# Kernel optimization log

Hardware: AMD Instinct MI355X
Metric: run time of the kernel (lower is better)

The kernel has to match this reference:

```python
import jax, jax.numpy as jnp
import numpy as np

B, IN_DIM, N, L = 8, 2, 512, 64
D_MODEL = 32
D_FF = 32          # must equal D_MODEL: output_bn is BatchNorm2d(d_model) applied to skip
DEPTH = 3          # blocks=3 * layers=1; dilation resets to 1 each block -> all dilations = 1
KS = 2             # temporal kernel size
EPS = 1e-5         # BatchNorm eps


def setup_inputs() -> dict:
    key = jax.random.key(0)
    ks = jax.random.split(key, 16)
    s = 0.1  # weight scale for numeric sanity
    x = jax.random.normal(ks[0], (B, IN_DIM, N, L), jnp.float32)
    a = jax.random.uniform(ks[1], (N, N), jnp.float32)
    adj = a / a.sum(axis=1, keepdims=True)  # row-stochastic diffusion matrix
    return {
        "x": x,
        "adj": adj,
        "Wstart": jax.random.normal(ks[2], (D_MODEL, IN_DIM), jnp.float32) * s,
        "bstart": jnp.zeros((D_MODEL,), jnp.float32),
        "Wf": jax.random.normal(ks[3], (DEPTH, D_MODEL, D_MODEL, KS), jnp.float32) * s,
        "bf": jnp.zeros((DEPTH, D_MODEL), jnp.float32),
        "Wg": jax.random.normal(ks[4], (DEPTH, D_MODEL, D_MODEL, KS), jnp.float32) * s,
        "bg": jnp.zeros((DEPTH, D_MODEL), jnp.float32),
        "Wskip": jax.random.normal(ks[5], (DEPTH, D_FF, D_MODEL), jnp.float32) * s,
        "bskip": jnp.zeros((DEPTH, D_FF), jnp.float32),
        "Wgc": jax.random.normal(ks[6], (DEPTH, D_MODEL, 3 * D_MODEL), jnp.float32) * s,
        "bgc": jnp.zeros((DEPTH, D_MODEL), jnp.float32),
        "gcbn_g": jnp.ones((DEPTH, D_MODEL), jnp.float32),
        "gcbn_b": jnp.zeros((DEPTH, D_MODEL), jnp.float32),
        "bn_g": jnp.ones((DEPTH, D_MODEL), jnp.float32),
        "bn_b": jnp.zeros((DEPTH, D_MODEL), jnp.float32),
        "obn_g": jnp.ones((D_MODEL,), jnp.float32),
        "obn_b": jnp.zeros((D_MODEL,), jnp.float32),
    }


def _c1x1(x, W, b):
    # Conv2d with (1,1) kernel == channel mixing. x: [b,c,n,l], W: [o,c]
    return jnp.einsum('bcnl,oc->bonl', x, W) + b[None, :, None, None]


def _dconv(x, W, b, d):
    # Conv2d kernel (1,2), dilation d along time (valid). W: [o,c,2]
    Lx = x.shape[-1]
    y = (jnp.einsum('bcnl,oc->bonl', x[..., :Lx - d], W[..., 0])
         + jnp.einsum('bcnl,oc->bonl', x[..., d:], W[..., 1]))
    return y + b[None, :, None, None]


def _bn(x, g, bta):
    # eval-mode BatchNorm2d: running_mean=0, running_var=1
    inv = g / jnp.sqrt(1.0 + EPS)
    return x * inv[None, :, None, None] + bta[None, :, None, None]


def reference(x, adj, Wstart, bstart, Wf, bf, Wg, bg, Wskip, bskip,
              Wgc, bgc, gcbn_g, gcbn_b, bn_g, bn_b, obn_g, obn_b):
    rf = 1 + DEPTH * (KS - 1)  # receptive field with dilation 1 per layer
    h = _c1x1(x, Wstart, bstart)
    if h.shape[-1] < rf:
        h = jnp.pad(h, ((0, 0), (0, 0), (0, 0), (rf - h.shape[-1], 0)))
    skip = None
    for i in range(DEPTH):
        residual = h
        filt = jnp.tanh(_dconv(h, Wf[i], bf[i], 1))
        gate = jax.nn.sigmoid(_dconv(h, Wg[i], bg[i], 1))
        h = filt * gate
        s = _c1x1(h, Wskip[i], bskip[i])
        skip = s if skip is None else s + skip[..., -s.shape[-1]:]
        if i == DEPTH - 1:
            break
        # order-2 graph diffusion: h, A h, A^2 h -> concat -> 1x1 conv -> BN (dropout: eval noop)
        x1 = jnp.einsum('bcnl,nm->bcml', h, adj)
        x2 = jnp.einsum('bcnl,nm->bcml', x1, adj)
        cat = jnp.concatenate([h, x1, x2], axis=1)
        g = _bn(_c1x1(cat, Wgc[i], bgc[i]), gcbn_g[i], gcbn_b[i])
        h = g + residual[..., -g.shape[-1]:]
        h = _bn(h, bn_g[i], bn_b[i])
    out = _bn(skip, obn_g, obn_b)
    return jnp.swapaxes(out, 1, 3)  # [B, L', N, C]
```

## Files before the change

### kernel.cpp

```cpp
#include <hip/hip_runtime.h>
#include <hip/hip_bf16.h>

#define B_     8
#define CIN_   2
#define N_     512
#define C_     32
#define L_     64
#define LOUT_  61
#define BUF_   ((size_t)(8*32*512*64))

typedef __hip_bfloat16 bf16;
typedef unsigned short ushort_t;
typedef unsigned int u32;
typedef __attribute__((ext_vector_type(8))) unsigned short us8;
typedef __attribute__((ext_vector_type(8))) short bf16x8;
typedef __attribute__((ext_vector_type(4))) float f32x4;

static __device__ __forceinline__ float bits2f(ushort_t u) {
    return __uint_as_float(((unsigned)u) << 16);
}
static __device__ __forceinline__ ushort_t f2bits(float v) {
    unsigned u = __float_as_uint(v);
    return (ushort_t)((u + 0x7fffu + ((u >> 16) & 1u)) >> 16);
}

static __device__ __forceinline__ void gload16(const ushort_t* g, ushort_t* l) {
    __builtin_amdgcn_global_load_lds(
        (const __attribute__((address_space(1))) unsigned int*)g,
        (__attribute__((address_space(3))) unsigned int*)l,
        16, 0, 0);
}

static __device__ __forceinline__ u32 swap1(u32 v) {
    return (u32)__builtin_amdgcn_update_dpp(0, (int)v, 0xB1, 0xF, 0xF, true);
}

__global__ void k_start(const float* __restrict__ x,
                        const float* __restrict__ Wst,
                        const float* __restrict__ bst,
                        ushort_t* __restrict__ h) {
    int idx = blockIdx.x * 256 + threadIdx.x;
    int l0 = (idx & 7) * 8;
    int n  = (idx >> 3) & 511;
    int o  = (idx >> 12) & 31;
    int b  = idx >> 17;
    float w0 = Wst[o * 2], w1 = Wst[o * 2 + 1], bb = bst[o];
    int xbase = (b * CIN_ * N_ + n) * L_ + l0;
    float va[8], vb[8];
    *(float4*)&va[0] = *(const float4*)(x + xbase);
    *(float4*)&va[4] = *(const float4*)(x + xbase + 4);
    *(float4*)&vb[0] = *(const float4*)(x + xbase + N_ * L_);
    *(float4*)&vb[4] = *(const float4*)(x + xbase + N_ * L_ + 4);
    us8 r;
    #pragma unroll
    for (int k = 0; k < 8; ++k) r[k] = f2bits(bb + va[k] * w0 + vb[k] * w1);
    *(us8*)(h + (size_t)idx * 8) = r;
}

__global__ void k_transA(const float* __restrict__ adj, ushort_t* __restrict__ adjT) {
    __shared__ float buf[64][65];
    int ti = blockIdx.x & 7;
    int tj = blockIdx.x >> 3;
    int t = threadIdx.x;
    for (int r = 0; r < 16; ++r) {
        int e = t + 256 * r;
        int rl = e >> 6, cl = e & 63;
        buf[rl][cl] = adj[(size_t)(ti * 64 + rl) * 512 + tj * 64 + cl];
    }
    __syncthreads();
    for (int r = 0; r < 16; ++r) {
        int e = t + 256 * r;
        int ml = e >> 6, nl = e & 63;
        adjT[(size_t)(tj * 64 + ml) * 512 + ti * 64 + nl] = f2bits(buf[nl][ml]);
    }
}

__global__ __launch_bounds__(256, 2) void k_sq(const ushort_t* __restrict__ adjT,
                                               ushort_t* __restrict__ adj2T) {
    __shared__ __align__(16) ushort_t lds2[8192];
    ushort_t* As = lds2;
    ushort_t* Bs = lds2 + 4096;
    int mt = blockIdx.x & 7, nc = blockIdx.x >> 3;
    int t = threadIdx.x, lane = t & 63, w = t >> 6;
    int la = lane & 15, q = lane >> 4;
    f32x4 acc[4];
    #pragma unroll
    for (int mi = 0; mi < 4; ++mi) acc[mi] = (f32x4)0.f;
    for (int p0 = 0; p0 < 512; p0 += 64) {
        __syncthreads();
        #pragma unroll
        for (int r = 0; r < 2; ++r) {
            int e = t + 256 * r, ml = e >> 3, oct = e & 7;
            int sw = ((oct + (ml >> 3)) & 7) << 3;
            *(us8*)(As + ml * 64 + sw) =
                *(const us8*)(adjT + (size_t)(mt * 64 + ml) * 512 + p0 + oct * 8);
            *(us8*)(Bs + ml * 64 + sw) =
                *(const us8*)(adjT + (size_t)(p0 + ml) * 512 + nc * 64 + oct * 8);
        }
        __syncthreads();
        #pragma unroll
        for (int ks = 0; ks < 2; ++ks) {
            bf16x8 a[4];
            #pragma unroll
            for (int mi = 0; mi < 4; ++mi) {
                int m = mi * 16 + la;
                int bl = (ks * 4 + q + (m >> 3)) & 7;
                a[mi] = *(const bf16x8*)(As + m * 64 + bl * 8);
            }
            bf16x8 bv;
            {
                int n = w * 16 + la;
                int rot = ((n >> 3) + ks * 4 + q) & 7;
                int col = rot * 8 + (n & 7);
                const ushort_t* p = Bs + (ks * 32 + q * 8) * 64 + col;
                #pragma unroll
                for (int j = 0; j < 8; ++j) bv[j] = (short)p[j * 64];
            }
            #pragma unroll
            for (int mi = 0; mi < 4; ++mi)
                acc[mi] = __builtin_amdgcn_mfma_f32_16x16x32_bf16(a[mi], bv, acc[mi], 0, 0, 0);
        }
    }
    __syncthreads();
    ushort_t* Ys = lds2;
    #pragma unroll
    for (int mi = 0; mi < 4; ++mi)
        #pragma unroll
        for (int r = 0; r < 4; ++r)
            Ys[(mi * 16 + q * 4 + r) * 72 + w * 16 + la] = f2bits(acc[mi][r]);
    __syncthreads();
    #pragma unroll
    for (int r = 0; r < 2; ++r) {
        int e = t + 256 * r, ml = e >> 3, oct = e & 7;
        us8 v = *(const us8*)(Ys + ml * 72 + oct * 8);
        *(us8*)(adj2T + (size_t)(mt * 64 + ml) * 512 + nc * 64 + oct * 8) = v;
    }
}

__global__ __launch_bounds__(256, 2) void k_gs_mfma(
        const ushort_t* __restrict__ h,
        const float* __restrict__ Wf, const float* __restrict__ bfp,
        const float* __restrict__ Wg, const float* __restrict__ bgp,
        const float* __restrict__ Wsk, const float* __restrict__ bsk,
        ushort_t* __restrict__ G, float* __restrict__ out,
        int off, int mode, int storeG,
        const float* __restrict__ og, const float* __restrict__ obb) {
    __shared__ __align__(16) ushort_t Hs[128 * 72];
    __shared__ __align__(16) ushort_t Asf[32 * 72];
    __shared__ __align__(16) ushort_t Asg[32 * 72];
    __shared__ __align__(16) ushort_t As2[32 * 40];
    __shared__ float bfv[32], bgv[32], bsv[32];
    int t = threadIdx.x;
    int b = blockIdx.x >> 7, n0 = (blockIdx.x & 127) * 4;
    int lane = t & 63, w = t >> 6;
    int la = lane & 15, q = lane >> 4;

    {
        int o = t >> 3, k8 = (t & 7) * 8;
        us8 vf, vg;
        #pragma unroll
        for (int i = 0; i < 8; ++i) {
            int k = k8 + i, c = k & 31, tap = k >> 5;
            vf[i] = f2bits(Wf[o * 64 + c * 2 + tap]);
            vg[i] = f2bits(Wg[o * 64 + c * 2 + tap]);
        }
        *(us8*)(Asf + o * 72 + k8) = vf;
        *(us8*)(Asg + o * 72 + k8) = vg;
        if (k8 < 32) {
            us8 vs;
            #pragma unroll
            for (int i = 0; i < 8; ++i) vs[i] = f2bits(Wsk[o * 32 + k8 + i]);
            *(us8*)(As2 + o * 40 + k8) = vs;
        }
        if (t < 32) { bfv[t] = bfp[t]; bgv[t] = bgp[t]; bsv[t] = bsk[t]; }
    }
    const ushort_t* hb = h + (size_t)(b * 32) * 512 * 64;
    #pragma unroll
    for (int r = 0; r < 4; ++r) {
        int e = t + 256 * r;
        int row = e >> 3, oct = e & 7;
        us8 v = *(const us8*)(hb + ((size_t)(row >> 2) * 512 + n0 + (row & 3)) * 64 + oct * 8);
        int sw = (oct + row + (row >> 5)) & 7;
        *(us8*)(Hs + row * 72 + sw * 8) = v;
    }
    {
        int row = t >> 1, hf = t & 1;
        *(uint2*)(Hs + row * 72 + 64 + hf * 4) = make_uint2(0u, 0u);
    }
    __syncthreads();

    bf16x8 af[2][2], ag[2][2];
    #pragma unroll
    for (int mt = 0; mt < 2; ++mt)
        #pragma unroll
        for (int ks = 0; ks < 2; ++ks) {
            af[mt][ks] = *(const bf16x8*)(Asf + (mt * 16 + la) * 72 + ks * 32 + q * 8);
            ag[mt][ks] = *(const bf16x8*)(Asg + (mt * 16 + la) * 72 + ks * 32 + q * 8);
        }

    f32x4 fa[2][4], ga[2][4];
    #pragma unroll
    for (int mt = 0; mt < 2; ++mt)
        #pragma unroll
        for (int ct = 0; ct < 4; ++ct) { fa[mt][ct] = (f32x4)0.f; ga[mt][ct] = (f32x4)0.f; }
    #pragma unroll
    for (int ct = 0; ct < 4; ++ct) {
        #pragma unroll
        for (int ks = 0; ks < 2; ++ks) {
            int le = ct * 16 + la + ks;
            bf16x8 bv;
            #pragma unroll
            for (int j = 0; j < 8; ++j) {
                int row = 32 * q + 4 * j + w;
                int pos = (le < 64) ? ((((le >> 3) + row + q) & 7) * 8 + (le & 7)) : le;
                bv[j] = (short)Hs[row * 72 + pos];
            }
            #pragma unroll
            for (int mt = 0; mt < 2; ++mt) {
                fa[mt][ct] = __builtin_amdgcn_mfma_f32_16x16x32_bf16(af[mt][ks], bv, fa[mt][ct], 0, 0, 0);
                ga[mt][ct] = __builtin_amdgcn_mfma_f32_16x16x32_bf16(ag[mt][ks], bv, ga[mt][ct], 0, 0, 0);
            }
        }
    }

    #pragma unroll
    for (int mt = 0; mt < 2; ++mt)
        #pragma unroll
        for (int ct = 0; ct < 4; ++ct)
            #pragma unroll
            for (int r = 0; r < 4; ++r) {
                int o = mt * 16 + q * 4 + r;
                float fv = fa[mt][ct][r] + bfv[o];
                float gv = ga[mt][ct][r] + bgv[o];
                float ef = __expf(2.f * fv);
                float act = (1.f - 2.f / (ef + 1.f)) * (1.f / (1.f + __expf(-gv)));
                int l = ct * 16 + la;
                int row = o * 4 + w;
                int sw = ((l >> 3) + row + (row >> 5)) & 7;
                Hs[row * 72 + sw * 8 + (l & 7)] = f2bits(act);
            }

    bf16x8 a2[2];
    a2[0] = *(const bf16x8*)(As2 + la * 40 + q * 8);
    a2[1] = *(const bf16x8*)(As2 + (16 + la) * 40 + q * 8);
    f32x4 sa[2][4];
    #pragma unroll
    for (int mt = 0; mt < 2; ++mt)
        #pragma unroll
        for (int ct = 0; ct < 4; ++ct) sa[mt][ct] = (f32x4)0.f;
    #pragma unroll
    for (int ct = 0; ct < 4; ++ct) {
        int le = ct * 16 + la + off;
        bf16x8 bv;
        #pragma unroll
        for (int j = 0; j < 8; ++j) {
            int row = 32 * q + 4 * j + w;
            int pos = (le < 64) ? ((((le >> 3) + row + q) & 7) * 8 + (le & 7)) : le;
            bv[j] = (short)Hs[row * 72 + pos];
        }
        sa[0][ct] = __builtin_amdgcn_mfma_f32_16x16x32_bf16(a2[0], bv, sa[0][ct], 0, 0, 0);
        sa[1][ct] = __builtin_amdgcn_mfma_f32_16x16x32_bf16(a2[1], bv, sa[1][ct], 0, 0, 0);
    }
    __syncthreads();

    if (storeG) {
        #pragma unroll
        for (int r = 0; r < 4; ++r) {
            int e = t + 256 * r;
            int row = e >> 3, oct = e & 7;
            int sw = (oct + row + (row >> 5)) & 7;
            us8 v = *(const us8*)(Hs + row * 72 + sw * 8);
            *(us8*)(G + ((size_t)(b * 32 + (row >> 2)) * 512 + n0 + (row & 3)) * 64 + oct * 8) = v;
        }
    }
    __syncthreads();

    float* St = (float*)Hs;
    const float rbn = rsqrtf(1.f + 1e-5f);
    #pragma unroll
    for (int half = 0; half < 2; ++half) {
        if ((w >> 1) == half) {
            #pragma unroll
            for (int mt = 0; mt < 2; ++mt)
                #pragma unroll
                for (int ct = 0; ct < 4; ++ct) {
                    int col = (w & 1) * 64 + ct * 16 + la;
                    int ob = mt * 16 + q * 4;
                    float4 sv = make_float4(sa[mt][ct][0] + bsv[ob],
                                            sa[mt][ct][1] + bsv[ob + 1],
                                            sa[mt][ct][2] + bsv[ob + 2],
                                            sa[mt][ct][3] + bsv[ob + 3]);
                    *(float4*)(St + col * 36 + ob) = sv;
                }
        }
        __syncthreads();
        {
            int col = t >> 1, o0 = (t & 1) * 16;
            int nr = half * 2 + (col >> 6), l = col & 63;
            if (l < LOUT_) {
                float* po = out + ((size_t)(b * LOUT_ + l) * 512 + n0 + nr) * 32 + o0;
                #pragma unroll
                for (int i = 0; i < 4; ++i) {
                    float4 s = *(float4*)(St + col * 36 + o0 + i * 4);
                    if (mode == 0) {
                        *(float4*)(po + i * 4) = s;
                    } else {
                        float4 old = *(float4*)(po + i * 4);
                        float4 vv = make_float4(old.x + s.x, old.y + s.y,
                                                old.z + s.z, old.w + s.w);
                        if (mode == 2) {
                            int ob = o0 + i * 4;
                            vv.x = vv.x * (og[ob] * rbn) + obb[ob];
                            vv.y = vv.y * (og[ob + 1] * rbn) + obb[ob + 1];
                            vv.z = vv.z * (og[ob + 2] * rbn) + obb[ob + 2];
                            vv.w = vv.w * (og[ob + 3] * rbn) + obb[ob + 3];
                        }
                        *(float4*)(po + i * 4) = vv;
                    }
                }
            }
        }
        __syncthreads();
    }
}

__global__ __launch_bounds__(256, 2) void k_diffuse2(
        const ushort_t* __restrict__ X, const ushort_t* __restrict__ adjT,
        const ushort_t* __restrict__ adj2T,
        ushort_t* __restrict__ Y1, ushort_t* __restrict__ Y2) {
    __shared__ __align__(16) ushort_t lds[32768];
    int cp = blockIdx.x & 15;
    int mt = (blockIdx.x >> 4) & 7;
    int b  = blockIdx.x >> 7;
    int t  = threadIdx.x;
    int lane = t & 63, w = t >> 6;
    int c_loc = w & 1, lh = w >> 1;
    int m0 = mt * 64;
    int la = lane & 15, q = lane >> 4;
    int p_ = la & 1;
    u32 sel = p_ ? 0x07060302u : 0x05040100u;
    const ushort_t* Xb = X + (size_t)(b * 32 + cp * 2) * 512 * 64;
    f32x4 acc1[4][2], acc2[4][2];
    #pragma unroll
    for (int mi = 0; mi < 4; ++mi)
        #pragma unroll
        for (int li = 0; li < 2; ++li) { acc1[mi][li] = (f32x4)0.f; acc2[mi][li] = (f32x4)0.f; }

    union U { u32 u[4]; bf16x8 v; };

    auto STAGE = [&](int n0, ushort_t* bb) {
        ushort_t* As1b = bb;
        ushort_t* As2b = bb + 4096;
        ushort_t* Xsb  = bb + 8192;
        #pragma unroll
        for (int r = 0; r < 2; ++r) {
            int e = t + 256 * r, ml = e >> 3, s = e & 7;
            int og = ((s - (ml >> 3)) & 7) * 8;
            gload16(adjT  + (size_t)(m0 + ml) * 512 + n0 + og, As1b + (size_t)e * 8);
            gload16(adj2T + (size_t)(m0 + ml) * 512 + n0 + og, As2b + (size_t)e * 8);
        }
        #pragma unroll
        for (int r = 0; r < 4; ++r) {
            int e = t + 256 * r;
            int cl = e >> 9, nl = (e >> 3) & 63, s = e & 7;
            int og = ((s - nl - (nl >> 3)) & 7) * 8;
            gload16(Xb + ((size_t)cl * 512 + n0 + nl) * 64 + og, Xsb + (size_t)e * 8);
        }
    };

    STAGE(0, lds);
    __syncthreads();

    for (int it = 0; it < 8; ++it) {
        ushort_t* cur = lds + (it & 1) * 16384;
        if (it < 7) STAGE((it + 1) * 64, lds + ((it + 1) & 1) * 16384);
        ushort_t* As1 = cur;
        ushort_t* As2 = cur + 4096;
        ushort_t* Xs  = cur + 8192;
        const ushort_t* xc = Xs + c_loc * 4096;
        #pragma unroll
        for (int ks = 0; ks < 2; ++ks) {
            bf16x8 a1[4], a2v[4];
            #pragma unroll
            for (int mi = 0; mi < 4; ++mi) {
                int m = mi * 16 + la;
                int bl = (ks * 4 + q + (m >> 3)) & 7;
                a1[mi]  = *(const bf16x8*)(As1 + m * 64 + bl * 8);
                a2v[mi] = *(const bf16x8*)(As2 + m * 64 + bl * 8);
            }
            bf16x8 bb[2];
            #pragma unroll
            for (int li = 0; li < 2; ++li) {
                int l2 = lh * 32 + li * 16 + (la & ~1);
                int r0 = ks * 32 + q * 8 + p_ * 4;
                int brot = ((l2 >> 3) + p_ * 4 + ks * 4 + q) & 7;
                u32 o0 = *(const u32*)(xc + (r0 + 0) * 64 + (((brot + 0) & 7) << 3) + (l2 & 7));
                u32 o1 = *(const u32*)(xc + (r0 + 1) * 64 + (((brot + 1) & 7) << 3) + (l2 & 7));
                u32 o2 = *(const u32*)(xc + (r0 + 2) * 64 + (((brot + 2) & 7) << 3) + (l2 & 7));
                u32 o3 = *(const u32*)(xc + (r0 + 3) * 64 + (((brot + 3) & 7) << 3) + (l2 & 7));
                u32 s0 = swap1(o0), s1 = swap1(o1), s2 = swap1(o2), s3 = swap1(o3);
                u32 lo0 = p_ ? s0 : o0, lo1 = p_ ? s1 : o1;
                u32 lo2 = p_ ? s2 : o2, lo3 = p_ ? s3 : o3;
                u32 hi0 = p_ ? o0 : s0, hi1 = p_ ? o1 : s1;
                u32 hi2 = p_ ? o2 : s2, hi3 = p_ ? o3 : s3;
                U u;
                u.u[0] = __builtin_amdgcn_perm(lo1, lo0, sel);
                u.u[1] = __builtin_amdgcn_perm(lo3, lo2, sel);
                u.u[2] = __builtin_amdgcn_perm(hi1, hi0, sel);
                u.u[3] = __builtin_amdgcn_perm(hi3, hi2, sel);
                bb[li] = u.v;
            }
            #pragma unroll
            for (int mi = 0; mi < 4; ++mi)
                #pragma unroll
                for (int li = 0; li < 2; ++li) {
                    acc1[mi][li] = __builtin_amdgcn_mfma_f32_16x16x32_bf16(a1[mi],  bb[li], acc1[mi][li], 0, 0, 0);
                    acc2[mi][li] = __builtin_amdgcn_mfma_f32_16x16x32_bf16(a2v[mi], bb[li], acc2[mi][li], 0, 0, 0);
                }
        }
        __syncthreads();
    }

    ushort_t* Ys = lds;
    #pragma unroll
    for (int pass = 0; pass < 2; ++pass) {
        __syncthreads();
        f32x4 (*src)[2] = pass ? acc2 : acc1;
        #pragma unroll
        for (int mi = 0; mi < 4; ++mi)
            #pragma unroll
            for (int li = 0; li < 2; ++li)
                #pragma unroll
                for (int r = 0; r < 4; ++r) {
                    int row = mi * 16 + q * 4 + r;
                    int col = lh * 32 + li * 16 + la;
                    Ys[c_loc * 4608 + row * 72 + col] = f2bits(src[mi][li][r]);
                }
        __syncthreads();
        ushort_t* Yo = pass ? Y2 : Y1;
        int c = t >> 7, mrem = t & 127;
        int m = mrem >> 1, lq = mrem & 1;
        #pragma unroll
        for (int r = 0; r < 4; ++r) {
            int l0 = lq * 32 + r * 8;
            us8 v = *(const us8*)(Ys + c * 4608 + m * 72 + l0);
            *(us8*)(Yo + ((size_t)(b * 32 + cp * 2 + c) * 512 + m0 + m) * 64 + l0) = v;
        }
    }
}

__global__ __launch_bounds__(256, 2) void k_gc3_mfma(
        ushort_t* __restrict__ G, const ushort_t* __restrict__ X1,
        const ushort_t* __restrict__ X2, const ushort_t* __restrict__ hres,
        const float* __restrict__ Wgc, const float* __restrict__ bgc,
        const float* __restrict__ gg, const float* __restrict__ gb,
        const float* __restrict__ bg2, const float* __restrict__ bb2) {
    __shared__ __align__(16) ushort_t cat[384 * 72];
    __shared__ __align__(16) ushort_t hr[128 * 64];
    __shared__ __align__(16) ushort_t Aw[32 * 104];
    __shared__ float prm[5][32];
    int t = threadIdx.x;
    int b = blockIdx.x >> 7, n0 = (blockIdx.x & 127) * 4;
    int lane = t & 63, w = t >> 6;
    int la = lane & 15, q = lane >> 4;

    #pragma unroll
    for (int r = 0; r < 12; ++r) {
        int e = t + 256 * r;
        int row = e >> 3, oct = e & 7;
        int k = row >> 2;
        const ushort_t* src = (k < 32) ? G : ((k < 64) ? X1 : X2);
        us8 v = *(const us8*)(src + ((size_t)(b * 32 + (k & 31)) * 512 + n0 + (row & 3)) * 64 + oct * 8);
        int sw = (oct + row + (row >> 5)) & 7;
        *(us8*)(cat + row * 72 + sw * 8) = v;
    }
    #pragma unroll
    for (int r = 0; r < 4; ++r) {
        int e = t + 256 * r;
        int row = e >> 3, oct = e & 7;
        us8 v = *(const us8*)(hres + ((size_t)(b * 32 + (row >> 2)) * 512 + n0 + (row & 3)) * 64 + oct * 8);
        *(us8*)(hr + row * 64 + oct * 8) = v;
    }
    for (int e = t; e < 384; e += 256) {
        int o = e / 12, oct = e % 12;
        us8 v;
        #pragma unroll
        for (int i = 0; i < 8; ++i) v[i] = f2bits(Wgc[o * 96 + oct * 8 + i]);
        *(us8*)(Aw + o * 104 + oct * 8) = v;
    }
    if (t < 32) {
        prm[0][t] = bgc[t]; prm[1][t] = gg[t]; prm[2][t] = gb[t];
        prm[3][t] = bg2[t]; prm[4][t] = bb2[t];
    }
    __syncthreads();

    bf16x8 a[2][3];
    #pragma unroll
    for (int mt = 0; mt < 2; ++mt)
        #pragma unroll
        for (int ks = 0; ks < 3; ++ks)
            a[mt][ks] = *(const bf16x8*)(Aw + (mt * 16 + la) * 104 + ks * 32 + q * 8);

    f32x4 acc[2][4];
    #pragma unroll
    for (int mt = 0; mt < 2; ++mt)
        #pragma unroll
        for (int ct = 0; ct < 4; ++ct) acc[mt][ct] = (f32x4)0.f;
    #pragma unroll
    for (int ct = 0; ct < 4; ++ct) {
        int le = ct * 16 + la;
        #pragma unroll
        for (int ks = 0; ks < 3; ++ks) {
            bf16x8 bv;
            #pragma unroll
            for (int j = 0; j < 8; ++j) {
                int row = (ks * 32 + q * 8 + j) * 4 + w;
                int sw = ((le >> 3) + row + (row >> 5)) & 7;
                bv[j] = (short)cat[row * 72 + sw * 8 + (le & 7)];
            }
            acc[0][ct] = __builtin_amdgcn_mfma_f32_16x16x32_bf16(a[0][ks], bv, acc[0][ct], 0, 0, 0);
            acc[1][ct] = __builtin_amdgcn_mfma_f32_16x16x32_bf16(a[1][ks], bv, acc[1][ct], 0, 0, 0);
        }
    }
    __syncthreads();

    const float rbn = rsqrtf(1.f + 1e-5f);
    #pragma unroll
    for (int mt = 0; mt < 2; ++mt)
        #pragma unroll
        for (int ct = 0; ct < 4; ++ct)
            #pragma unroll
            for (int r = 0; r < 4; ++r) {
                int o = mt * 16 + q * 4 + r;
                int l = ct * 16 + la;
                float v = acc[mt][ct][r] + prm[0][o];
                v = v * (prm[1][o] * rbn) + prm[2][o];
                float res = (l < 63) ? bits2f(hr[(o * 4 + w) * 64 + l + 1]) : 0.f;
                v = (v + res) * (prm[3][o] * rbn) + prm[4][o];
                int row = o * 4 + w;
                int sw = ((l >> 3) + row + (row >> 5)) & 7;
                cat[row * 72 + sw * 8 + (l & 7)] = f2bits(v);
            }
    __syncthreads();
    #pragma unroll
    for (int r = 0; r < 4; ++r) {
        int e = t + 256 * r;
        int row = e >> 3, oct = e & 7;
        int sw = (oct + row + (row >> 5)) & 7;
        us8 v = *(const us8*)(cat + row * 72 + sw * 8);
        *(us8*)(G + ((size_t)(b * 32 + (row >> 2)) * 512 + n0 + (row & 3)) * 64 + oct * 8) = v;
    }
}

extern "C" void kernel_launch(void* const* d_in, const int* in_sizes, int n_in,
                              void* d_out, int out_size, void* d_ws, size_t ws_size,
                              hipStream_t stream) {
    const float* x      = (const float*)d_in[0];
    const float* adj    = (const float*)d_in[1];
    const float* Wstart = (const float*)d_in[2];
    const float* bstart = (const float*)d_in[3];
    const float* Wf     = (const float*)d_in[4];
    const float* bf_    = (const float*)d_in[5];
    const float* Wg     = (const float*)d_in[6];
    const float* bg     = (const float*)d_in[7];
    const float* Wskip  = (const float*)d_in[8];
    const float* bskip  = (const float*)d_in[9];
    const float* Wgc    = (const float*)d_in[10];
    const float* bgc    = (const float*)d_in[11];
    const float* gcbn_g = (const float*)d_in[12];
    const float* gcbn_b = (const float*)d_in[13];
    const float* bn_g   = (const float*)d_in[14];
    const float* bn_b   = (const float*)d_in[15];
    const float* obn_g  = (const float*)d_in[16];
    const float* obn_b  = (const float*)d_in[17];
    float* out = (float*)d_out;

    ushort_t* P0    = (ushort_t*)d_ws;
    ushort_t* P1    = P0 + BUF_;
    ushort_t* P2    = P1 + BUF_;
    ushort_t* P3    = P2 + BUF_;
    ushort_t* adjT  = P3 + BUF_;
    ushort_t* adj2T = adjT + 512 * 512;

    k_transA<<<64, 256, 0, stream>>>(adj, adjT);
    k_sq<<<64, 256, 0, stream>>>(adjT, adj2T);
    k_start<<<4096, 256, 0, stream>>>(x, Wstart, bstart, P0);

    ushort_t* h  = P0;
    ushort_t* Gb = P1;
    for (int i = 0; i < 3; ++i) {
        int mode = (i == 0) ? 0 : ((i == 2) ? 2 : 1);
        k_gs_mfma<<<1024, 256, 0, stream>>>(h, Wf + i * 2048, bf_ + i * 32,
                                            Wg + i * 2048, bg + i * 32,
                                            Wskip + i * 1024, bskip + i * 32,
                                            Gb, out, 2 - i, mode, (i < 2) ? 1 : 0,
                                            obn_g, obn_b);
        if (i == 2) break;
        k_diffuse2<<<1024, 256, 0, stream>>>(Gb, adjT, adj2T, P2, P3);
        k_gc3_mfma<<<1024, 256, 0, stream>>>(Gb, P2, P3, h,
                                             Wgc + i * 3072, bgc + i * 32,
                                             gcbn_g + i * 32, gcbn_b + i * 32,
                                             bn_g + i * 32, bn_b + i * 32);
        ushort_t* tmp = h; h = Gb; Gb = tmp;
    }
}
```

Baseline: 308.9 us.

## Halve per-block node tile in gated-skip kernel to raise occupancy

The gated temporal conv + skip kernel now processes 2 nodes per block instead of 4, doubling the grid to 2048 blocks. Each wave handles half the time columns for one node, which shrinks the accumulator arrays and the LDS footprint, and the launch-bounds hint is raised to 6 blocks per CU. The skip output store no longer needs two staged halves. In exchange, the weight matrices are loaded into LDS by twice as many blocks, extra barriers are added, and each block does less work to amortize its fixed setup.

```diff
diff --git a/kernel.cpp b/kernel.cpp
--- a/kernel.cpp
+++ b/kernel.cpp
@@ -137,7 +137,7 @@
     }
 }
 
-__global__ __launch_bounds__(256, 2) void k_gs_mfma(
+__global__ __launch_bounds__(256, 6) void k_gs_mfma(
         const ushort_t* __restrict__ h,
         const float* __restrict__ Wf, const float* __restrict__ bfp,
         const float* __restrict__ Wg, const float* __restrict__ bgp,
@@ -145,14 +145,16 @@
         ushort_t* __restrict__ G, float* __restrict__ out,
         int off, int mode, int storeG,
         const float* __restrict__ og, const float* __restrict__ obb) {
-    __shared__ __align__(16) ushort_t Hs[128 * 72];
-    __shared__ __align__(16) ushort_t Asf[32 * 72];
-    __shared__ __align__(16) ushort_t Asg[32 * 72];
-    __shared__ __align__(16) ushort_t As2[32 * 40];
+    __shared__ __align__(16) ushort_t lds[10496];
+    ushort_t* Hs  = lds;
+    ushort_t* Asf = lds + 4608;
+    ushort_t* Asg = lds + 6912;
+    ushort_t* As2 = lds + 9216;
     __shared__ float bfv[32], bgv[32], bsv[32];
     int t = threadIdx.x;
-    int b = blockIdx.x >> 7, n0 = (blockIdx.x & 127) * 4;
+    int b = blockIdx.x >> 8, n0 = (blockIdx.x & 255) * 2;
     int lane = t & 63, w = t >> 6;
+    int ng = w & 1, cg = w >> 1;
     int la = lane & 15, q = lane >> 4;
 
     {
@@ -176,14 +178,14 @@
     }
     const ushort_t* hb = h + (size_t)(b * 32) * 512 * 64;
     #pragma unroll
-    for (int r = 0; r < 4; ++r) {
+    for (int r = 0; r < 2; ++r) {
         int e = t + 256 * r;
         int row = e >> 3, oct = e & 7;
-        us8 v = *(const us8*)(hb + ((size_t)(row >> 2) * 512 + n0 + (row & 3)) * 64 + oct * 8);
+        us8 v = *(const us8*)(hb + ((size_t)(row >> 1) * 512 + n0 + (row & 1)) * 64 + oct * 8);
         int sw = (oct + row + (row >> 5)) & 7;
         *(us8*)(Hs + row * 72 + sw * 8) = v;
     }
-    {
+    if (t < 128) {
         int row = t >> 1, hf = t & 1;
         *(uint2*)(Hs + row * 72 + 64 + hf * 4) = make_uint2(0u, 0u);
     }
@@ -198,129 +200,126 @@
             ag[mt][ks] = *(const bf16x8*)(Asg + (mt * 16 + la) * 72 + ks * 32 + q * 8);
         }
 
-    f32x4 fa[2][4], ga[2][4];
-    #pragma unroll
-    for (int mt = 0; mt < 2; ++mt)
-        #pragma unroll
-        for (int ct = 0; ct < 4; ++ct) { fa[mt][ct] = (f32x4)0.f; ga[mt][ct] = (f32x4)0.f; }
-    #pragma unroll
-    for (int ct = 0; ct < 4; ++ct) {
+    f32x4 fa[2][2], ga[2][2];
+    #pragma unroll
+    for (int mt = 0; mt < 2; ++mt)
+        #pragma unroll
+        for (int cl = 0; cl < 2; ++cl) { fa[mt][cl] = (f32x4)0.f; ga[mt][cl] = (f32x4)0.f; }
+    #pragma unroll
+    for (int cl = 0; cl < 2; ++cl) {
+        int ct = cg * 2 + cl;
         #pragma unroll
         for (int ks = 0; ks < 2; ++ks) {
             int le = ct * 16 + la + ks;
             bf16x8 bv;
             #pragma unroll
             for (int j = 0; j < 8; ++j) {
-                int row = 32 * q + 4 * j + w;
-                int pos = (le < 64) ? ((((le >> 3) + row + q) & 7) * 8 + (le & 7)) : le;
+                int row = (q * 8 + j) * 2 + ng;
+                int pos = (le < 64) ? ((((le >> 3) + row + (row >> 5)) & 7) * 8 + (le & 7)) : le;
                 bv[j] = (short)Hs[row * 72 + pos];
             }
             #pragma unroll
             for (int mt = 0; mt < 2; ++mt) {
-                fa[mt][ct] = __builtin_amdgcn_mfma_f32_16x16x32_bf16(af[mt][ks], bv, fa[mt][ct], 0, 0, 0);
-                ga[mt][ct] = __builtin_amdgcn_mfma_f32_16x16x32_bf16(ag[mt][ks], bv, ga[mt][ct], 0, 0, 0);
-            }
-        }
-    }
-
-    #pragma unroll
-    for (int mt = 0; mt < 2; ++mt)
-        #pragma unroll
-        for (int ct = 0; ct < 4; ++ct)
+                fa[mt][cl] = __builtin_amdgcn_mfma_f32_16x16x32_bf16(af[mt][ks], bv, fa[mt][cl], 0, 0, 0);
+                ga[mt][cl] = __builtin_amdgcn_mfma_f32_16x16x32_bf16(ag[mt][ks], bv, ga[mt][cl], 0, 0, 0);
+            }
+        }
+    }
+    __syncthreads();
+
+    #pragma unroll
+    for (int mt = 0; mt < 2; ++mt)
+        #pragma unroll
+        for (int cl = 0; cl < 2; ++cl)
             #pragma unroll
             for (int r = 0; r < 4; ++r) {
                 int o = mt * 16 + q * 4 + r;
-                float fv = fa[mt][ct][r] + bfv[o];
-                float gv = ga[mt][ct][r] + bgv[o];
+                float fv = fa[mt][cl][r] + bfv[o];
+                float gv = ga[mt][cl][r] + bgv[o];
                 float ef = __expf(2.f * fv);
                 float act = (1.f - 2.f / (ef + 1.f)) * (1.f / (1.f + __expf(-gv)));
-                int l = ct * 16 + la;
-                int row = o * 4 + w;
+                int l = (cg * 2 + cl) * 16 + la;
+                int row = o * 2 + ng;
                 int sw = ((l >> 3) + row + (row >> 5)) & 7;
                 Hs[row * 72 + sw * 8 + (l & 7)] = f2bits(act);
             }
+    __syncthreads();
 
     bf16x8 a2[2];
     a2[0] = *(const bf16x8*)(As2 + la * 40 + q * 8);
     a2[1] = *(const bf16x8*)(As2 + (16 + la) * 40 + q * 8);
-    f32x4 sa[2][4];
-    #pragma unroll
-    for (int mt = 0; mt < 2; ++mt)
-        #pragma unroll
-        for (int ct = 0; ct < 4; ++ct) sa[mt][ct] = (f32x4)0.f;
-    #pragma unroll
-    for (int ct = 0; ct < 4; ++ct) {
-        int le = ct * 16 + la + off;
+    f32x4 sa[2][2];
+    #pragma unroll
+    for (int mt = 0; mt < 2; ++mt)
+        #pragma unroll
+        for (int cl = 0; cl < 2; ++cl) sa[mt][cl] = (f32x4)0.f;
+    #pragma unroll
+    for (int cl = 0; cl < 2; ++cl) {
+        int le = (cg * 2 + cl) * 16 + la + off;
         bf16x8 bv;
         #pragma unroll
         for (int j = 0; j < 8; ++j) {
-            int row = 32 * q + 4 * j + w;
-            int pos = (le < 64) ? ((((le >> 3) + row + q) & 7) * 8 + (le & 7)) : le;
+            int row = (q * 8 + j) * 2 + ng;
+            int pos = (le < 64) ? ((((le >> 3) + row + (row >> 5)) & 7) * 8 + (le & 7)) : le;
             bv[j] = (short)Hs[row * 72 + pos];
         }
-        sa[0][ct] = __builtin_amdgcn_mfma_f32_16x16x32_bf16(a2[0], bv, sa[0][ct], 0, 0, 0);
-        sa[1][ct] = __builtin_amdgcn_mfma_f32_16x16x32_bf16(a2[1], bv, sa[1][ct], 0, 0, 0);
+        sa[0][cl] = __builtin_amdgcn_mfma_f32_16x16x32_bf16(a2[0], bv, sa[0][cl], 0, 0, 0);
+        sa[1][cl] = __builtin_amdgcn_mfma_f32_16x16x32_bf16(a2[1], bv, sa[1][cl], 0, 0, 0);
     }
     __syncthreads();
 
     if (storeG) {
         #pragma unroll
-        for (int r = 0; r < 4; ++r) {
+        for (int r = 0; r < 2; ++r) {
             int e = t + 256 * r;
             int row = e >> 3, oct = e & 7;
             int sw = (oct + row + (row >> 5)) & 7;
             us8 v = *(const us8*)(Hs + row * 72 + sw * 8);
-            *(us8*)(G + ((size_t)(b * 32 + (row >> 2)) * 512 + n0 + (row & 3)) * 64 + oct * 8) = v;
-        }
-    }
-    __syncthreads();
-
-    float* St = (float*)Hs;
+            *(us8*)(G + ((size_t)(b * 32 + (row >> 1)) * 512 + n0 + (row & 1)) * 64 + oct * 8) = v;
+        }
+    }
+    __syncthreads();
+
+    float* St = (float*)lds;
     const float rbn = rsqrtf(1.f + 1e-5f);
     #pragma unroll
-    for (int half = 0; half < 2; ++half) {
-        if ((w >> 1) == half) {
-            #pragma unroll
-            for (int mt = 0; mt < 2; ++mt)
-                #pragma unroll
-                for (int ct = 0; ct < 4; ++ct) {
-                    int col = (w & 1) * 64 + ct * 16 + la;
-                    int ob = mt * 16 + q * 4;
-                    float4 sv = make_float4(sa[mt][ct][0] + bsv[ob],
-                                            sa[mt][ct][1] + bsv[ob + 1],
-                                            sa[mt][ct][2] + bsv[ob + 2],
-                                            sa[mt][ct][3] + bsv[ob + 3]);
-                    *(float4*)(St + col * 36 + ob) = sv;
+    for (int mt = 0; mt < 2; ++mt)
+        #pragma unroll
+        for (int cl = 0; cl < 2; ++cl) {
+            int col = ng * 64 + (cg * 2 + cl) * 16 + la;
+            int ob = mt * 16 + q * 4;
+            float4 sv = make_float4(sa[mt][cl][0] + bsv[ob],
+                                    sa[mt][cl][1] + bsv[ob + 1],
+                                    sa[mt][cl][2] + bsv[ob + 2],
+                                    sa[mt][cl][3] + bsv[ob + 3]);
+            *(float4*)(St + col * 36 + ob) = sv;
+        }
+    __syncthreads();
+    {
+        int col = t >> 1, o0 = (t & 1) * 16;
+        int nr = col >> 6, l = col & 63;
+        if (l < LOUT_) {
+            float* po = out + ((size_t)(b * LOUT_ + l) * 512 + n0 + nr) * 32 + o0;
+            #pragma unroll
+            for (int i = 0; i < 4; ++i) {
+                float4 s = *(float4*)(St + col * 36 + o0 + i * 4);
+                if (mode == 0) {
+                    *(float4*)(po + i * 4) = s;
+                } else {
+                    float4 old = *(float4*)(po + i * 4);
+                    float4 vv = make_float4(old.x + s.x, old.y + s.y,
+                                            old.z + s.z, old.w + s.w);
+                    if (mode == 2) {
+                        int ob = o0 + i * 4;
+                        vv.x = vv.x * (og[ob] * rbn) + obb[ob];
+                        vv.y = vv.y * (og[ob + 1] * rbn) + obb[ob + 1];
+                        vv.z = vv.z * (og[ob + 2] * rbn) + obb[ob + 2];
+                        vv.w = vv.w * (og[ob + 3] * rbn) + obb[ob + 3];
+                    }
+                    *(float4*)(po + i * 4) = vv;
                 }
-        }
-        __syncthreads();
-        {
-            int col = t >> 1, o0 = (t & 1) * 16;
-            int nr = half * 2 + (col >> 6), l = col & 63;
-            if (l < LOUT_) {
-                float* po = out + ((size_t)(b * LOUT_ + l) * 512 + n0 + nr) * 32 + o0;
-                #pragma unroll
-                for (int i = 0; i < 4; ++i) {
-                    float4 s = *(float4*)(St + col * 36 + o0 + i * 4);
-                    if (mode == 0) {
-                        *(float4*)(po + i * 4) = s;
-                    } else {
-                        float4 old = *(float4*)(po + i * 4);
-                        float4 vv = make_float4(old.x + s.x, old.y + s.y,
-                                                old.z + s.z, old.w + s.w);
-                        if (mode == 2) {
-                            int ob = o0 + i * 4;
-                            vv.x = vv.x * (og[ob] * rbn) + obb[ob];
-                            vv.y = vv.y * (og[ob + 1] * rbn) + obb[ob + 1];
-                            vv.z = vv.z * (og[ob + 2] * rbn) + obb[ob + 2];
-                            vv.w = vv.w * (og[ob + 3] * rbn) + obb[ob + 3];
-                        }
-                        *(float4*)(po + i * 4) = vv;
-                    }
-                }
-            }
-        }
-        __syncthreads();
+            }
+        }
     }
 }
 
@@ -590,7 +589,7 @@
     ushort_t* Gb = P1;
     for (int i = 0; i < 3; ++i) {
         int mode = (i == 0) ? 0 : ((i == 2) ? 2 : 1);
-        k_gs_mfma<<<1024, 256, 0, stream>>>(h, Wf + i * 2048, bf_ + i * 32,
+        k_gs_mfma<<<2048, 256, 0, stream>>>(h, Wf + i * 2048, bf_ + i * 32,
                                             Wg + i * 2048, bg + i * 32,
                                             Wskip + i * 1024, bskip + i * 32,
                                             Gb, out, 2 - i, mode, (i < 2) ? 1 : 0,
```

After: 320.7 us. 1.04x slower.
